# Kernel tuning notes

Measured on AMD Instinct MI355X. Metric: run time of the kernel, lower is better.

The kernel has to match this reference:

```python
import jax, jax.numpy as jnp
import numpy as np

N, E, B = 100_000, 1_600_000, 100      # nodes, edges, graphs
IN, HID, OUT = 128, 128, 128           # feature dims
N_PER = N // B                          # nodes per graph


def _w(k, shape, fan_in):
    return jax.random.normal(k, shape, jnp.float32) / np.sqrt(fan_in).astype(np.float32)


def setup_inputs() -> dict:
    key = jax.random.key(0)
    ks = jax.random.split(key, 10)
    x = jax.random.normal(ks[0], (N, IN), jnp.float32)
    edge_index = jax.random.randint(ks[1], (2, E), 0, N, jnp.int32)
    batch_vector = jnp.repeat(jnp.arange(B, dtype=jnp.int32), N_PER)  # sorted graph ids
    local_target_node_idx = jax.random.randint(ks[2], (B,), 0, N_PER, jnp.int32)
    return {
        "x": x,
        "edge_index": edge_index,
        "local_target_node_idx": local_target_node_idx,
        "batch_vector": batch_vector,
        "num_graphs": B,
        # SAGEConv1: lin_l (neighbor, with bias) + lin_r (root, no bias)
        "W1_l": _w(ks[3], (HID, IN), IN), "b1_l": jnp.zeros((HID,), jnp.float32),
        "W1_r": _w(ks[4], (HID, IN), IN),
        # SAGEConv2
        "W2_l": _w(ks[5], (OUT, HID), HID), "b2_l": jnp.zeros((OUT,), jnp.float32),
        "W2_r": _w(ks[6], (OUT, HID), HID),
        # classifier MLP
        "Wc1": _w(ks[7], (OUT // 2, OUT), OUT), "bc1": jnp.zeros((OUT // 2,), jnp.float32),
        "Wc2": _w(ks[8], (1, OUT // 2), OUT // 2), "bc2": jnp.zeros((1,), jnp.float32),
    }


def sage_conv(x, src, dst, W_l, b_l, W_r):
    """PyG SAGEConv (aggr='mean', root_weight=True): lin_l(mean_j x_j) + lin_r(x_i)."""
    n = x.shape[0]
    msgs = x[src]                                                 # [E, d] gather
    agg = jax.ops.segment_sum(msgs, dst, num_segments=n)          # scatter-add at targets
    cnt = jax.ops.segment_sum(jnp.ones((src.shape[0],), x.dtype), dst, num_segments=n)
    mean = agg / jnp.maximum(cnt, 1.0)[:, None]                   # isolated nodes -> 0
    return mean @ W_l.T + b_l + x @ W_r.T


def reference(x, edge_index, local_target_node_idx, batch_vector, num_graphs,
              W1_l, b1_l, W1_r, W2_l, b2_l, W2_r, Wc1, bc1, Wc2, bc2):
    src, dst = edge_index[0], edge_index[1]
    h = jax.nn.relu(sage_conv(x, src, dst, W1_l, b1_l, W1_r))
    h = jax.nn.relu(sage_conv(h, src, dst, W2_l, b2_l, W2_r))
    # offsets = bincount.cumsum - bincount (start index of each graph)
    counts = jax.ops.segment_sum(jnp.ones_like(batch_vector), batch_vector,
                                 num_segments=num_graphs)
    offsets = jnp.cumsum(counts) - counts
    t = h[local_target_node_idx + offsets]                        # [B, OUT]
    z = jax.nn.relu(t @ Wc1.T + bc1)
    return z @ Wc2.T + bc2                                        # [B, 1]
```

## Files before the change

### kernel.cpp

```cpp
#include <hip/hip_runtime.h>
#include <hip/hip_bf16.h>
#include <stdint.h>

#define CAPA 16384
#define CAPN 16640
#define PA_CAP 1024
#define PC_CAP 512

__global__ void k_batch_start(const int* __restrict__ bv, int N, int* __restrict__ start) {
    int i = blockIdx.x * blockDim.x + threadIdx.x;
    if (i < N) {
        int b = bv[i];
        if (i == 0 || bv[i - 1] != b) start[b] = i;
    }
}

__global__ void k_tgt_mark(const int* __restrict__ start, const int* __restrict__ local_t,
                           int B, int* __restrict__ tgt, int* __restrict__ tgtmark,
                           int* __restrict__ mark1) {
    int b = blockIdx.x * blockDim.x + threadIdx.x;
    if (b < B) {
        int g = local_t[b] + start[b];
        tgt[b] = g;
        tgtmark[g] = b + 1;
        mark1[g] = 1;
    }
}

__global__ __launch_bounds__(256) void k_passA(
    const int* __restrict__ src, const int* __restrict__ dst, int E,
    const int* __restrict__ tgtmark, int* __restrict__ mark1,
    int2* __restrict__ listA, int* __restrict__ cnt) {
    __shared__ int2 buf[PA_CAP];
    __shared__ int lcnt, gbase;
    int t = threadIdx.x;
    if (t == 0) lcnt = 0;
    __syncthreads();
    int per = (E + gridDim.x - 1) / gridDim.x;
    int lo = blockIdx.x * per;
    int hi = lo + per; if (hi > E) hi = E;
    for (int i = lo + t; i < hi; i += blockDim.x) {
        int tm = tgtmark[dst[i]];
        if (tm) {
            int s = src[i];
            mark1[s] = 1;
            int p = atomicAdd(&lcnt, 1);
            if (p < PA_CAP) buf[p] = make_int2(tm - 1, s);
        }
    }
    __syncthreads();
    int n = lcnt; if (n > PA_CAP) n = PA_CAP;
    if (t == 0) gbase = atomicAdd(&cnt[0], n);
    __syncthreads();
    for (int p = t; p < n; p += blockDim.x) {
        int g = gbase + p;
        if (g < CAPA) listA[g] = buf[p];
    }
}

__global__ __launch_bounds__(256) void k_compact(
    const int* __restrict__ mark1, int N,
    int* __restrict__ cidmap, int* __restrict__ anodes, int* __restrict__ cnt) {
    __shared__ int buf[PC_CAP];
    __shared__ int lcnt, gbase;
    int t = threadIdx.x;
    if (t == 0) lcnt = 0;
    __syncthreads();
    int per = (N + gridDim.x - 1) / gridDim.x;
    int lo = blockIdx.x * per;
    int hi = lo + per; if (hi > N) hi = N;
    for (int i = lo + t; i < hi; i += blockDim.x) {
        if (mark1[i]) {
            int p = atomicAdd(&lcnt, 1);
            if (p < PC_CAP) buf[p] = i;
        }
    }
    __syncthreads();
    int n = lcnt; if (n > PC_CAP) n = PC_CAP;
    if (t == 0) gbase = atomicAdd(&cnt[1], n);
    __syncthreads();
    for (int p = t; p < n; p += blockDim.x) {
        int g = gbase + p;
        if (g < CAPN) { anodes[g] = buf[p]; cidmap[buf[p]] = g + 1; }
    }
}

__global__ __launch_bounds__(256) void k_scatter(
    const float* __restrict__ x, const int* __restrict__ src,
    const int* __restrict__ dst, int E, const int* __restrict__ cidmap,
    float* __restrict__ meanacc, int* __restrict__ cntN) {
    int lane = threadIdx.x & 63;
    int wid = (blockIdx.x * blockDim.x + threadIdx.x) >> 6;
    int nw = (gridDim.x * blockDim.x) >> 6;
    const float2* xp = (const float2*)x;
    for (long long base = (long long)wid * 64; base < E; base += (long long)nw * 64) {
        int i = (int)base + lane;
        int c = 0, s = 0;
        if (i < E) {
            c = cidmap[dst[i]];
            s = src[i];
        }
        unsigned long long mask = __ballot(c != 0);
        while (mask) {
            int l = __ffsll(mask) - 1;
            int cc = __shfl(c, l) - 1;
            int ss = __shfl(s, l);
            float2 v = xp[(size_t)ss * 64 + lane];
            unsafeAtomicAdd(&meanacc[(size_t)cc * 128 + 2 * lane], v.x);
            unsafeAtomicAdd(&meanacc[(size_t)cc * 128 + 2 * lane + 1], v.y);
            if (lane == 0) atomicAdd(&cntN[cc], 1);
            mask &= mask - 1;
        }
    }
}

__global__ void k_transpose2(const float* __restrict__ A, const float* __restrict__ B,
                             float* __restrict__ AT, float* __restrict__ BT) {
    int i = blockIdx.x * blockDim.x + threadIdx.x;
    if (i < 128 * 128) {
        int o = i >> 7, k = i & 127;
        AT[k * 128 + o] = A[i];
        BT[k * 128 + o] = B[i];
    }
}

__global__ __launch_bounds__(256) void k_lin_compact(
    const float* __restrict__ x, const int* __restrict__ anodes,
    const float* __restrict__ meanacc, const int* __restrict__ cntN,
    const int* __restrict__ cnt,
    const float* __restrict__ WlT, const float* __restrict__ WrT,
    const float* __restrict__ bias, float* __restrict__ out) {
    int nA = cnt[1]; if (nA > CAPN) nA = CAPN;
    int row0 = blockIdx.x * 64;
    if (row0 >= nA) return;
    __shared__ float ms[64 * 129];
    __shared__ float xs[64 * 129];
    int t = threadIdx.x;

    const float4* mp = (const float4*)meanacc;
    const float4* xp = (const float4*)x;
#pragma unroll
    for (int i = 0; i < 8; i++) {
        int slot = t + i * 256;
        int r = slot >> 5, c4 = slot & 31;
        int gr = row0 + r;
        float4 mv = {0, 0, 0, 0}, xv = {0, 0, 0, 0};
        if (gr < nA) {
            int node = anodes[gr];
            int dcount = cntN[gr];
            float inv = 1.0f / (float)((dcount > 0) ? dcount : 1);
            mv = mp[(size_t)gr * 32 + c4];
            mv.x *= inv; mv.y *= inv; mv.z *= inv; mv.w *= inv;
            xv = xp[(size_t)node * 32 + c4];
        }
        int lb = r * 129 + c4 * 4;
        ms[lb] = mv.x; ms[lb + 1] = mv.y; ms[lb + 2] = mv.z; ms[lb + 3] = mv.w;
        xs[lb] = xv.x; xs[lb + 1] = xv.y; xs[lb + 2] = xv.z; xs[lb + 3] = xv.w;
    }
    __syncthreads();

    int q = __builtin_amdgcn_readfirstlane(t >> 6);
    int lane = t & 63;
    int ob = q * 32;

    float acc[32];
#pragma unroll
    for (int o = 0; o < 32; o++) acc[o] = bias[ob + o];

    for (int k = 0; k < 128; k++) {
        float m  = ms[lane * 129 + k];
        float xx = xs[lane * 129 + k];
        const float* wl = WlT + k * 128 + ob;
        const float* wr = WrT + k * 128 + ob;
#pragma unroll
        for (int o = 0; o < 32; o++) {
            acc[o] += m * wl[o] + xx * wr[o];
        }
    }

    int gr = row0 + lane;
    if (gr < nA) {
        float4* op = (float4*)(out + (size_t)gr * 128 + ob);
#pragma unroll
        for (int o4 = 0; o4 < 8; o4++) {
            float4 v;
            v.x = fmaxf(acc[o4 * 4 + 0], 0.f);
            v.y = fmaxf(acc[o4 * 4 + 1], 0.f);
            v.z = fmaxf(acc[o4 * 4 + 2], 0.f);
            v.w = fmaxf(acc[o4 * 4 + 3], 0.f);
            op[o4] = v;
        }
    }
}

__global__ __launch_bounds__(128) void k_targets(
    const float* __restrict__ h1c, const int* __restrict__ tgt,
    const int* __restrict__ cidmap, const int2* __restrict__ listA,
    const int* __restrict__ cnt,
    const float* __restrict__ W2l, const float* __restrict__ b2,
    const float* __restrict__ W2r,
    const float* __restrict__ Wc1, const float* __restrict__ bc1,
    const float* __restrict__ Wc2, const float* __restrict__ bc2,
    float* __restrict__ out) {
    __shared__ int match[4096];
    __shared__ int mcount;
    __shared__ float mean_s[128], hg_s[128], h2_s[128], z_s[64];
    int b = blockIdx.x;
    int t = threadIdx.x;
    if (t == 0) mcount = 0;
    __syncthreads();

    int nAe = cnt[0]; if (nAe > CAPA) nAe = CAPA;
    for (int e = t; e < nAe; e += 128) {
        int2 ent = listA[e];
        if (ent.x == b) {
            int p = atomicAdd(&mcount, 1);
            if (p < 4096) match[p] = ent.y;
        }
    }
    __syncthreads();
    int m = mcount; if (m > 4096) m = 4096;

    float acc = 0.f;
    for (int j = 0; j < m; j++) {
        int c = cidmap[match[j]] - 1;
        if (c >= 0) acc += h1c[(size_t)c * 128 + t];
    }
    mean_s[t] = acc / (float)((m > 0) ? m : 1);
    int gc = cidmap[tgt[b]] - 1;
    hg_s[t] = (gc >= 0) ? h1c[(size_t)gc * 128 + t] : 0.f;
    __syncthreads();

    float v = b2[t];
    for (int k = 0; k < 128; k++) {
        v += mean_s[k] * W2l[t * 128 + k] + hg_s[k] * W2r[t * 128 + k];
    }
    h2_s[t] = fmaxf(v, 0.f);
    __syncthreads();

    if (t < 64) {
        float z = bc1[t];
        for (int k = 0; k < 128; k++) z += h2_s[k] * Wc1[t * 128 + k];
        z_s[t] = fmaxf(z, 0.f);
    }
    __syncthreads();

    if (t == 0) {
        float o = bc2[0];
        for (int j = 0; j < 64; j++) o += z_s[j] * Wc2[j];
        out[b] = o;
    }
}


extern "C" void kernel_launch(void* const* d_in, const int* in_sizes, int n_in,
                              void* d_out, int out_size, void* d_ws, size_t ws_size,
                              hipStream_t stream) {
    const float* x       = (const float*)d_in[0];
    const int*   ei      = (const int*)d_in[1];
    const int*   local_t = (const int*)d_in[2];
    const int*   bv      = (const int*)d_in[3];
    const float* W1l = (const float*)d_in[5];
    const float* b1  = (const float*)d_in[6];
    const float* W1r = (const float*)d_in[7];
    const float* W2l = (const float*)d_in[8];
    const float* b2  = (const float*)d_in[9];
    const float* W2r = (const float*)d_in[10];
    const float* Wc1 = (const float*)d_in[11];
    const float* bc1 = (const float*)d_in[12];
    const float* Wc2 = (const float*)d_in[13];
    const float* bc2 = (const float*)d_in[14];
    float* out = (float*)d_out;

    int N = in_sizes[0] / 128;
    int E = in_sizes[1] / 2;
    int B = in_sizes[2];
    const int* src  = ei;
    const int* dstp = ei + E;

    char* w = (char*)d_ws;
    auto alloc = [&](size_t bytes) -> void* {
        void* p = (void*)w;
        w += (bytes + 255) & ~((size_t)255);
        return p;
    };
    char* zbase = w;
    int*   tgtmark = (int*)alloc((size_t)N * 4);
    int*   mark1   = (int*)alloc((size_t)N * 4);
    int*   cidmap  = (int*)alloc((size_t)N * 4);
    int*   cnt     = (int*)alloc(64);
    int*   cntN    = (int*)alloc((size_t)CAPN * 4);
    float* meanacc = (float*)alloc((size_t)CAPN * 128 * 4);
    size_t zbytes = (size_t)(w - zbase);
    int*   bstart = (int*)alloc((size_t)B * 4);
    int*   tgt    = (int*)alloc((size_t)B * 4);
    int*   anodes = (int*)alloc((size_t)CAPN * 4);
    int2*  listA  = (int2*)alloc((size_t)CAPA * 8);
    float* W1lT   = (float*)alloc(128 * 128 * 4);
    float* W1rT   = (float*)alloc(128 * 128 * 4);
    float* h1c    = (float*)alloc((size_t)CAPN * 128 * 4);

    hipMemsetAsync(zbase, 0, zbytes, stream);

    k_batch_start<<<(N + 255) / 256, 256, 0, stream>>>(bv, N, bstart);
    k_tgt_mark<<<(B + 63) / 64, 64, 0, stream>>>(bstart, local_t, B, tgt, tgtmark, mark1);
    k_passA<<<512, 256, 0, stream>>>(src, dstp, E, tgtmark, mark1, listA, cnt);
    k_compact<<<256, 256, 0, stream>>>(mark1, N, cidmap, anodes, cnt);
    k_transpose2<<<(128 * 128 + 255) / 256, 256, 0, stream>>>(W1l, W1r, W1lT, W1rT);
    k_scatter<<<2048, 256, 0, stream>>>(x, src, dstp, E, cidmap, meanacc, cntN);
    k_lin_compact<<<CAPN / 64, 256, 0, stream>>>(x, anodes, meanacc, cntN, cnt,
                                                 W1lT, W1rT, b1, h1c);
    k_targets<<<B, 128, 0, stream>>>(h1c, tgt, cidmap, listA, cnt, W2l, b2, W2r,
                                     Wc1, bc1, Wc2, bc2, out);
}
```

Before: 248.3 us.

## Restructure compact linear kernel to one output column per thread, two rows per block

The first-layer linear kernel changes from 64 rows per block, with each thread computing 32 outputs for one row, to 2 rows per block with each thread computing a single output column. The aim is more blocks and lower register pressure, so occupancy and latency hiding improve. In exchange each weight element is read from global/L2 once per 2 rows instead of once per 64 rows. That greatly increases weight traffic, and the inner loop now does scalar loads with far less reuse.

```diff
diff --git a/kernel.cpp b/kernel.cpp
--- a/kernel.cpp
+++ b/kernel.cpp
@@ -6,6 +6,7 @@
 #define CAPN 16640
 #define PA_CAP 1024
 #define PC_CAP 512
+#define LIN_ROWS 2
 
 __global__ void k_batch_start(const int* __restrict__ bv, int N, int* __restrict__ start) {
     int i = blockIdx.x * blockDim.x + threadIdx.x;
@@ -131,66 +132,31 @@
     const float* __restrict__ WlT, const float* __restrict__ WrT,
     const float* __restrict__ bias, float* __restrict__ out) {
     int nA = cnt[1]; if (nA > CAPN) nA = CAPN;
-    int row0 = blockIdx.x * 64;
+    int row0 = blockIdx.x * LIN_ROWS;
     if (row0 >= nA) return;
-    __shared__ float ms[64 * 129];
-    __shared__ float xs[64 * 129];
-    int t = threadIdx.x;
-
-    const float4* mp = (const float4*)meanacc;
-    const float4* xp = (const float4*)x;
-#pragma unroll
-    for (int i = 0; i < 8; i++) {
-        int slot = t + i * 256;
-        int r = slot >> 5, c4 = slot & 31;
-        int gr = row0 + r;
-        float4 mv = {0, 0, 0, 0}, xv = {0, 0, 0, 0};
-        if (gr < nA) {
-            int node = anodes[gr];
-            int dcount = cntN[gr];
-            float inv = 1.0f / (float)((dcount > 0) ? dcount : 1);
-            mv = mp[(size_t)gr * 32 + c4];
-            mv.x *= inv; mv.y *= inv; mv.z *= inv; mv.w *= inv;
-            xv = xp[(size_t)node * 32 + c4];
-        }
-        int lb = r * 129 + c4 * 4;
-        ms[lb] = mv.x; ms[lb + 1] = mv.y; ms[lb + 2] = mv.z; ms[lb + 3] = mv.w;
-        xs[lb] = xv.x; xs[lb + 1] = xv.y; xs[lb + 2] = xv.z; xs[lb + 3] = xv.w;
-    }
-    __syncthreads();
-
-    int q = __builtin_amdgcn_readfirstlane(t >> 6);
-    int lane = t & 63;
-    int ob = q * 32;
-
-    float acc[32];
-#pragma unroll
-    for (int o = 0; o < 32; o++) acc[o] = bias[ob + o];
-
+    __shared__ float ms[LIN_ROWS][128];
+    __shared__ float xs[LIN_ROWS][128];
+    int t = threadIdx.x;
+    int r = t >> 7, o = t & 127;
+    int gr = row0 + r;
+    if (gr < nA) {
+        int node = anodes[gr];
+        int d = cntN[gr];
+        float inv = 1.0f / (float)((d > 0) ? d : 1);
+        ms[r][o] = meanacc[(size_t)gr * 128 + o] * inv;
+        xs[r][o] = x[(size_t)node * 128 + o];
+    } else {
+        ms[r][o] = 0.f;
+        xs[r][o] = 0.f;
+    }
+    __syncthreads();
+
+    float acc = bias[o];
+#pragma unroll 4
     for (int k = 0; k < 128; k++) {
-        float m  = ms[lane * 129 + k];
-        float xx = xs[lane * 129 + k];
-        const float* wl = WlT + k * 128 + ob;
-        const float* wr = WrT + k * 128 + ob;
-#pragma unroll
-        for (int o = 0; o < 32; o++) {
-            acc[o] += m * wl[o] + xx * wr[o];
-        }
-    }
-
-    int gr = row0 + lane;
-    if (gr < nA) {
-        float4* op = (float4*)(out + (size_t)gr * 128 + ob);
-#pragma unroll
-        for (int o4 = 0; o4 < 8; o4++) {
-            float4 v;
-            v.x = fmaxf(acc[o4 * 4 + 0], 0.f);
-            v.y = fmaxf(acc[o4 * 4 + 1], 0.f);
-            v.z = fmaxf(acc[o4 * 4 + 2], 0.f);
-            v.w = fmaxf(acc[o4 * 4 + 3], 0.f);
-            op[o4] = v;
-        }
-    }
+        acc += ms[r][k] * WlT[k * 128 + o] + xs[r][k] * WrT[k * 128 + o];
+    }
+    if (gr < nA) out[(size_t)gr * 128 + o] = fmaxf(acc, 0.f);
 }
 
 __global__ __launch_bounds__(128) void k_targets(
@@ -308,8 +274,8 @@
     k_compact<<<256, 256, 0, stream>>>(mark1, N, cidmap, anodes, cnt);
     k_transpose2<<<(128 * 128 + 255) / 256, 256, 0, stream>>>(W1l, W1r, W1lT, W1rT);
     k_scatter<<<2048, 256, 0, stream>>>(x, src, dstp, E, cidmap, meanacc, cntN);
-    k_lin_compact<<<CAPN / 64, 256, 0, stream>>>(x, anodes, meanacc, cntN, cnt,
-                                                 W1lT, W1rT, b1, h1c);
+    k_lin_compact<<<CAPN / LIN_ROWS, 256, 0, stream>>>(x, anodes, meanacc, cntN, cnt,
+                                                       W1lT, W1rT, b1, h1c);
     k_targets<<<B, 128, 0, stream>>>(h1c, tgt, cidmap, listA, cnt, W2l, b2, W2r,
                                      Wc1, bc1, Wc2, bc2, out);
 }
```

After: 209.3 us. 15.7% less time.
